# Kernel tuning notes

Measured on AMD Instinct MI355X. Metric: run time of the kernel, lower is better.

The kernel has to match this reference:

```python
import jax, jax.numpy as jnp
import numpy as np

DIM = 1024
HID = 2048
E = 8
K = 2
EPS = 1e-9


def setup_inputs() -> dict:
    key = jax.random.key(0)
    ks = jax.random.split(key, 6)
    scale = 0.02
    return {
        "x": jax.random.normal(ks[0], (4, 2048, DIM), jnp.float32),
        "gate_w": jax.random.normal(ks[1], (DIM, E), jnp.float32) * scale,
        "gate_b": jnp.zeros((E,), jnp.float32),
        # stacked expert weights: leading dim = expert index
        "w1": jax.random.normal(ks[2], (E, DIM, HID), jnp.float32) * scale,
        "b1": jnp.zeros((E, HID), jnp.float32),
        "w2": jax.random.normal(ks[3], (E, DIM, HID), jnp.float32) * scale,
        "b2": jnp.zeros((E, HID), jnp.float32),
        "w3": jax.random.normal(ks[4], (E, HID, DIM), jnp.float32) * scale,
        "b3": jnp.zeros((E, DIM), jnp.float32),
    }


def reference(x, gate_w, gate_b, w1, b1, w2, b2, w3, b3):
    # x: (b, s, d)
    logits = x @ gate_w + gate_b                      # (b, s, E)
    scores = jax.nn.softmax(logits, axis=-1)
    topk_scores, topk_idx = jax.lax.top_k(scores, K)  # (b, s, K)

    usage = scores.mean(axis=(0, 1))                  # (E,)
    load_balance_loss = jnp.sum(usage * jnp.log(usage + EPS))

    # per-expert combine weight: score if expert in top-k else 0  -> (b, s, E)
    onehot = jax.nn.one_hot(topk_idx, E, dtype=x.dtype)            # (b, s, K, E)
    combine = jnp.sum(topk_scores[..., None] * onehot, axis=2)     # (b, s, E)

    out = jnp.zeros_like(x)
    for e in range(E):  # small fixed loop over experts
        gate = jax.nn.sigmoid(x @ w2[e] + b2[e])      # (b, s, H)
        h = (x @ w1[e] + b1[e]) * gate                # SwiGLU hidden
        out = out + combine[..., e:e + 1] * (h @ w3[e] + b3[e])
    return out, load_balance_loss
```

## Files before the change

### kernel.cpp

```cpp
#include <hip/hip_runtime.h>
#include <hip/hip_bf16.h>
#include <math.h>

#define N_TOK 8192
#define DIM   1024
#define HID   2048
#define NE    8
#define NT1   16
#define NT2   32
#define NB1   16
#define NB2   4
#define MAXT  72
#define PANEL1_SH ((size_t)(128 * 256 * 8))
#define PANEL3_SH ((size_t)(256 * 256 * 8))
#define XBLK_SH   ((size_t)(128 * 128 * 8))
#define HBLK_SH   ((size_t)(256 * 128 * 8))

typedef __attribute__((ext_vector_type(8))) short short8;
typedef __attribute__((ext_vector_type(4))) float f32x4;
typedef unsigned short us;

__device__ __forceinline__ us f2bf(float f) {
    unsigned int u = __builtin_bit_cast(unsigned int, f);
    unsigned int r = (u + 0x7fffu + ((u >> 16) & 1u)) >> 16;
    return (us)r;
}

__device__ __forceinline__ float bf2f(us v) {
    unsigned int u = ((unsigned int)v) << 16;
    return __builtin_bit_cast(float, u);
}

__device__ __forceinline__ void gl_lds16(const us* g, us* l) {
    __builtin_amdgcn_global_load_lds(
        (const __attribute__((address_space(1))) void*)g,
        (__attribute__((address_space(3))) void*)l, 16, 0, 0);
}

#define VMW4 asm volatile("s_waitcnt vmcnt(4)" ::: "memory")
#define VMW0 asm volatile("s_waitcnt vmcnt(0)" ::: "memory")
#define BARM asm volatile("s_barrier" ::: "memory")
#define PRIO1 __builtin_amdgcn_s_setprio(1)
#define PRIO0 __builtin_amdgcn_s_setprio(0)

__global__ __launch_bounds__(256) void gate_compute(
    const float* __restrict__ x, const float* __restrict__ gw, const float* __restrict__ gb,
    int* __restrict__ sel, float2* __restrict__ wpair, float* __restrict__ usage_part)
{
    const int lane = threadIdx.x & 63;
    const int tok = blockIdx.x * 4 + (threadIdx.x >> 6);

    __shared__ float su[NE];
    if (threadIdx.x < NE) su[threadIdx.x] = 0.f;
    __syncthreads();

    float acc[NE];
#pragma unroll
    for (int e = 0; e < NE; e++) acc[e] = 0.f;

    const float* xr = x + (size_t)tok * DIM;
    for (int d = lane; d < DIM; d += 64) {
        float xv = xr[d];
        const float4* g4 = (const float4*)(gw + (size_t)d * NE);
        float4 ga = g4[0], gc = g4[1];
        acc[0] = fmaf(xv, ga.x, acc[0]);
        acc[1] = fmaf(xv, ga.y, acc[1]);
        acc[2] = fmaf(xv, ga.z, acc[2]);
        acc[3] = fmaf(xv, ga.w, acc[3]);
        acc[4] = fmaf(xv, gc.x, acc[4]);
        acc[5] = fmaf(xv, gc.y, acc[5]);
        acc[6] = fmaf(xv, gc.z, acc[6]);
        acc[7] = fmaf(xv, gc.w, acc[7]);
    }
#pragma unroll
    for (int e = 0; e < NE; e++) {
#pragma unroll
        for (int off = 32; off > 0; off >>= 1)
            acc[e] += __shfl_xor(acc[e], off);
    }

    if (lane == 0) {
        float lg[NE], p[NE];
        float mx = -1e30f;
#pragma unroll
        for (int e = 0; e < NE; e++) { lg[e] = acc[e] + gb[e]; mx = fmaxf(mx, lg[e]); }
        float s = 0.f;
#pragma unroll
        for (int e = 0; e < NE; e++) { p[e] = __expf(lg[e] - mx); s += p[e]; }
        float inv = 1.f / s;
#pragma unroll
        for (int e = 0; e < NE; e++) p[e] *= inv;
#pragma unroll
        for (int e = 0; e < NE; e++) atomicAdd(&su[e], p[e]);

        int e1 = 0; float v1 = p[0];
#pragma unroll
        for (int e = 1; e < NE; e++) if (p[e] > v1) { v1 = p[e]; e1 = e; }
        int e2 = -1; float v2 = -1e30f;
#pragma unroll
        for (int e = 0; e < NE; e++) if (e != e1 && p[e] > v2) { v2 = p[e]; e2 = e; }

        sel[tok] = e1 | (e2 << 4);
        wpair[tok] = make_float2(v1, v2);
    }
    __syncthreads();
    if (threadIdx.x < NE) usage_part[blockIdx.x * NE + threadIdx.x] = su[threadIdx.x];
}

__global__ __launch_bounds__(256) void scan_kernel(
    const int* __restrict__ sel, const float2* __restrict__ wpair,
    int* __restrict__ counts, int* __restrict__ lists, float* __restrict__ wlist)
{
    const int e = blockIdx.x;
    const int t = threadIdx.x;
    const int base_tok = t * 32;

    unsigned selm = 0, km = 0;
#pragma unroll
    for (int i = 0; i < 32; i++) {
        int s = sel[base_tok + i];
        int e1 = s & 15, e2 = (s >> 4) & 15;
        if (e1 == e) selm |= (1u << i);
        else if (e2 == e) { selm |= (1u << i); km |= (1u << i); }
    }
    const int myc = __popc(selm);

    __shared__ int tot[256];
    tot[t] = myc;
    __syncthreads();
#pragma unroll
    for (int d = 1; d < 256; d <<= 1) {
        int v = (t >= d) ? tot[t - d] : 0;
        __syncthreads();
        tot[t] += v;
        __syncthreads();
    }
    int pos = tot[t] - myc;
    if (t == 255) counts[e] = tot[255];

    for (int i = 0; i < 32; i++) {
        if (selm & (1u << i)) {
            int tok = base_tok + i;
            int k = (km >> i) & 1;
            lists[e * N_TOK + pos] = tok * 2 + k;
            float2 wp = wpair[tok];
            wlist[e * N_TOK + pos] = k ? wp.y : wp.x;
            pos++;
        }
    }
}

__global__ __launch_bounds__(256) void usage_reduce(
    const float* __restrict__ part, float* __restrict__ usage)
{
    const int t = threadIdx.x;
    const int e = t & 7, chunk = t >> 3;
    float s = 0.f;
    for (int b = chunk; b < 2048; b += 32) s += part[b * NE + e];
    __shared__ float red[256];
    red[t] = s;
    __syncthreads();
#pragma unroll
    for (int step = 128; step >= 8; step >>= 1) {
        if (t < step) red[t] += red[t + step];
        __syncthreads();
    }
    if (t < NE) usage[t] = red[t];
}

__global__ void loss_kernel(const float* __restrict__ usage, float* __restrict__ out_loss)
{
    if (threadIdx.x == 0) {
        float l = 0.f;
        for (int e = 0; e < NE; e++) {
            float u = usage[e] / (float)N_TOK;
            l += u * logf(u + 1e-9f);
        }
        *out_loss = l;
    }
}

__global__ void prefix_kernel(const int* __restrict__ counts,
                              int* __restrict__ base_exact, int* __restrict__ ntiles,
                              int* __restrict__ tmap_e, int* __restrict__ tmap_m0)
{
    if (threadIdx.x == 0) {
        int bx = 0, nt = 0;
        for (int e = 0; e < NE; e++) {
            base_exact[e] = bx;
            for (int m0 = 0; m0 < counts[e]; m0 += 256) {
                tmap_e[nt] = e; tmap_m0[nt] = m0; nt++;
            }
            bx += counts[e];
        }
        ntiles[0] = nt;
    }
}

__global__ __launch_bounds__(256) void inv_kernel(
    const int* __restrict__ counts, const int* __restrict__ lists,
    const int* __restrict__ base_exact, int* __restrict__ inv)
{
    const int e = blockIdx.y;
    const int idx = blockIdx.x * 256 + threadIdx.x;
    if (idx < counts[e]) inv[lists[e * N_TOK + idx]] = base_exact[e] + idx;
}

__global__ __launch_bounds__(256) void xgather_kernel(
    const float* __restrict__ x,
    const int* __restrict__ counts, const int* __restrict__ lists,
    const int* __restrict__ base_exact,
    us* __restrict__ Xg)
{
    __shared__ int toks[128];
    __shared__ int bexs[NE], cnts[NE];
    const int t = threadIdx.x;
    if (t < NE) { bexs[t] = base_exact[t]; cnts[t] = counts[t]; }
    __syncthreads();
    if (t < 128) {
        int gpos = blockIdx.x * 128 + t;
        int e = 0;
#pragma unroll
        for (int k = 1; k < NE; k++) if (gpos >= bexs[k]) e = k;
        int idx = gpos - bexs[e];
        int tok = (idx < cnts[e]) ? (lists[e * N_TOK + idx] >> 1) : 0;
        toks[t] = tok;
    }
    __syncthreads();

    us* op = Xg + (size_t)blockIdx.x * XBLK_SH;
    const int rr = t & 127;
    const int ch = t >> 7;
    const int tok = toks[rr];
#pragma unroll
    for (int it = 0; it < 64; it++) {
        int c = it * 2 + ch;
        const float4* src = (const float4*)(x + (size_t)tok * DIM + c * 8);
        float4 a = src[0], b = src[1];
        short8 v;
        v[0] = (short)f2bf(a.x); v[1] = (short)f2bf(a.y);
        v[2] = (short)f2bf(a.z); v[3] = (short)f2bf(a.w);
        v[4] = (short)f2bf(b.x); v[5] = (short)f2bf(b.y);
        v[6] = (short)f2bf(b.z); v[7] = (short)f2bf(b.w);
        *(short8*)(op + (size_t)(c * 128 + rr) * 8) = v;
    }
}

__global__ __launch_bounds__(256) void wswz12_kernel(
    const float* __restrict__ w1, const float* __restrict__ w2, us* __restrict__ out)
{
    const int e = blockIdx.z, nbx = blockIdx.y, gs = blockIdx.x;
    us* op = out + ((size_t)e * NB1 + nbx) * PANEL1_SH + (size_t)gs * 8 * 256 * 8;
    const float* w1e = w1 + (size_t)e * DIM * HID;
    const float* w2e = w2 + (size_t)e * DIM * HID;
    const int t = threadIdx.x;
#pragma unroll
    for (int it = 0; it < 8; it++) {
        int idx = it * 256 + t;
        int g = idx >> 8, row = idx & 255;
        int col = nbx * 128 + (row & 127);
        const float* src = (row < 128 ? w1e : w2e) + (size_t)((gs * 8 + g) * 8) * HID + col;
        short8 v;
#pragma unroll
        for (int s = 0; s < 8; s++) v[s] = (short)f2bf(src[(size_t)s * HID]);
        *(short8*)(op + (size_t)idx * 8) = v;
    }
}

__global__ __launch_bounds__(256) void wswz3_kernel(
    const float* __restrict__ w3, us* __restrict__ out)
{
    const int e = blockIdx.z, nbx = blockIdx.y, gs = blockIdx.x;
    us* op = out + ((size_t)e * NB2 + nbx) * PANEL3_SH + (size_t)gs * 8 * 256 * 8;
    const float* w3e = w3 + (size_t)e * HID * DIM;
    const int t = threadIdx.x;
#pragma unroll
    for (int it = 0; it < 8; it++) {
        int idx = it * 256 + t;
        int g = idx >> 8, row = idx & 255;
        int col = nbx * 256 + row;
        const float* src = w3e + (size_t)((gs * 8 + g) * 8) * DIM + col;
        short8 v;
#pragma unroll
        for (int s = 0; s < 8; s++) v[s] = (short)f2bf(src[(size_t)s * DIM]);
        *(short8*)(op + (size_t)idx * 8) = v;
    }
}

#define ABUF(b) ((us*)(SM + (b)*32768))
#define BBUF(b) ((us*)(SM + 65536 + (b)*32768))

#define AF_READ(b, h) do {                                               \
    _Pragma("unroll")                                                    \
    for (int mi = 0; mi < 8; mi++)                                       \
        af[mi] = *(const short8*)(ABUF(b) + ((h)*1024 + kc*256 + Mw + mi*16 + fr)*8); \
} while (0)
#define BF_READ4(b, h) do {                                              \
    _Pragma("unroll")                                                    \
    for (int j = 0; j < 4; j++)                                          \
        bfv[j] = *(const short8*)(BBUF(b) + ((h)*1024 + kc*256 + Nw + j*16 + fr)*8); \
} while (0)
#define CLUST4 do {                                                      \
    PRIO1;                                                               \
    _Pragma("unroll")                                                    \
    for (int j = 0; j < 4; j++) {                                        \
        _Pragma("unroll")                                                \
        for (int mi = 0; mi < 8; mi++)                                   \
            acc[mi][j] = __builtin_amdgcn_mfma_f32_16x16x32_bf16(        \
                af[mi], bfv[j], acc[mi][j], 0, 0, 0);                    \
    }                                                                    \
    PRIO0;                                                               \
} while (0)

__global__ __launch_bounds__(512, 2) void ffn1_mfma_kernel(
    const us* __restrict__ Xg, const us* __restrict__ W12sw,
    const float* __restrict__ b1, const float* __restrict__ b2,
    const int* __restrict__ counts, const int* __restrict__ base_exact,
    const int* __restrict__ ntiles, const int* __restrict__ tmap_e, const int* __restrict__ tmap_m0,
    us* __restrict__ Hsw)
{
    const int hw = blockIdx.x;
    const int ix = hw >> 3;
    const int nbx = ((hw & 7) << 1) | (ix & 1);
    const int by  = ix >> 1;
    if (by >= ntiles[0]) return;
    const int e  = tmap_e[by];
    const int m0 = tmap_m0[by];
    const int cnt = counts[e];
    const int bex = base_exact[e];

    __shared__ __align__(16) unsigned char SM[132096];

    const int t = threadIdx.x;
    const int lane = t & 63, wv = t >> 6;
    const int wr = wv >> 2, wc = wv & 3;
    const int Mw = wr * 128, Nw = wc * 64;
    const int fr = lane & 15, kc = lane >> 4;

    float bb[4];
    {
        const float* bsrc = (wc < 2) ? b1 : b2;
#pragma unroll
        for (int ni = 0; ni < 4; ni++)
            bb[ni] = bsrc[e * HID + nbx * 128 + (wc & 1) * 64 + ni * 16 + fr];
    }
    __syncthreads();

    const int c0 = wv * 128 + lane;
    const int c1 = c0 + 64;
    const int RA0 = min(bex + m0 + (c0 & 255), N_TOK * 2 - 1);
    const int RA1 = min(bex + m0 + (c1 & 255), N_TOK * 2 - 1);
    const us* ApA = Xg + (size_t)(RA0 >> 7) * XBLK_SH + (size_t)(c0 >> 8) * 1024 + (RA0 & 127) * 8;
    const us* ApB = Xg + (size_t)(RA1 >> 7) * XBLK_SH + (size_t)(c1 >> 8) * 1024 + (RA1 & 127) * 8;
    const us* Wp = W12sw + ((size_t)e * NB1 + nbx) * PANEL1_SH;
    const int dbase = wv * 128 * 8;

    f32x4 acc[8][4];
    const f32x4 fz = {0.f, 0.f, 0.f, 0.f};
#pragma unroll
    for (int i = 0; i < 8; i++)
#pragma unroll
        for (int j = 0; j < 4; j++) acc[i][j] = fz;

    #define STAGE_A(b, tile, h) do {                                             \
        gl_lds16(ApA + (size_t)((tile)*8 + (h)*4) * 1024, ABUF(b) + ((h)*1024)*8 + dbase); \
        gl_lds16(ApB + (size_t)((tile)*8 + (h)*4) * 1024, ABUF(b) + ((h)*1024 + 64)*8 + dbase); \
    } while (0)
    #define STAGE_B(b, tile, h) do {                                             \
        const us* s_ = Wp + ((size_t)(tile)*2048 + (h)*1024) * 8;                \
        gl_lds16(s_ + (size_t)c0 * 8, BBUF(b) + ((h)*1024)*8 + dbase);           \
        gl_lds16(s_ + (size_t)c1 * 8, BBUF(b) + ((h)*1024 + 64)*8 + dbase);      \
    } while (0)

    short8 af[8], bfv[4];

    STAGE_A(0, 0, 0); STAGE_B(0, 0, 0); STAGE_A(0, 0, 1); STAGE_B(0, 0, 1);
    VMW4; BARM;

    for (int tl = 0; tl < NT1; ++tl) {
        const int b = tl & 1, nb = b ^ 1;
        const bool more = (tl + 1 < NT1);
        AF_READ(b, 0); BF_READ4(b, 0);
        if (more) { STAGE_A(nb, tl + 1, 0); STAGE_B(nb, tl + 1, 0); VMW4; } else { VMW0; }
        BARM; CLUST4; BARM;
        AF_READ(b, 1); BF_READ4(b, 1);
        if (more) { STAGE_A(nb, tl + 1, 1); STAGE_B(nb, tl + 1, 1); VMW4; }
        BARM; CLUST4; BARM;
    }
    #undef STAGE_A
    #undef STAGE_B

    float* G = (float*)SM;
    if (wc >= 2) {
        const int cp = wc - 2;
#pragma unroll
        for (int ni = 0; ni < 4; ni++) {
            int c2 = cp * 64 + ni * 16 + fr;
#pragma unroll
            for (int mi = 0; mi < 8; mi++) {
#pragma unroll
                for (int j = 0; j < 4; j++) {
                    int m = mi * 16 + kc * 4 + j;
                    float g = 1.f / (1.f + __expf(-(acc[mi][ni][j] + bb[ni])));
                    G[(wr * 128 + c2) * 129 + m] = g;
                }
            }
        }
    }
    __syncthreads();
    if (wc < 2) {
#pragma unroll
        for (int ni = 0; ni < 4; ni++) {
            int c2 = wc * 64 + ni * 16 + fr;
            int ch = nbx * 128 + c2;
            size_t cb = (size_t)(ch >> 3) * 128 * 8 + (ch & 7);
#pragma unroll
            for (int mi = 0; mi < 8; mi++) {
#pragma unroll
                for (int j = 0; j < 4; j++) {
                    int m = mi * 16 + kc * 4 + j;
                    int rl = wr * 128 + m;
                    if (m0 + rl >= cnt) continue;
                    float h = (acc[mi][ni][j] + bb[ni]) * G[(wr * 128 + c2) * 129 + m];
                    int R = bex + m0 + rl;
                    Hsw[(size_t)(R >> 7) * HBLK_SH + cb + (size_t)(R & 127) * 8] = f2bf(h);
                }
            }
        }
    }
}

__global__ __launch_bounds__(512, 2) void ffn2_mfma_kernel(
    const us* __restrict__ Hsw, const us* __restrict__ W3sw, const float* __restrict__ b3,
    const int* __restrict__ counts, const int* __restrict__ base_exact,
    const int* __restrict__ ntiles, const int* __restrict__ tmap_e, const int* __restrict__ tmap_m0,
    const float* __restrict__ wts,
    us* __restrict__ Pb)
{
    const int hw = blockIdx.x;
    const int xcd = hw & 7;
    const int ix = hw >> 3;
    const int nbx = xcd & 3;
    const int by = (ix << 1) | (xcd >> 2);
    if (by >= ntiles[0]) return;
    const int e  = tmap_e[by];
    const int m0 = tmap_m0[by];
    const int cnt = counts[e];
    const int bex = base_exact[e];

    __shared__ __align__(16) unsigned char SM[132096];
    float* rowwt = (float*)(SM + 131072);

    const int t = threadIdx.x;
    if (t < 256) {
        int idx = m0 + t;
        rowwt[t] = (idx < cnt) ? wts[e * N_TOK + idx] : 0.f;
    }

    const int lane = t & 63, wv = t >> 6;
    const int wr = wv >> 2, wc = wv & 3;
    const int Mw = wr * 128, Nw = wc * 64;
    const int fr = lane & 15, kc = lane >> 4;

    float bb3[4];
#pragma unroll
    for (int ni = 0; ni < 4; ni++)
        bb3[ni] = b3[e * DIM + nbx * 256 + wc * 64 + ni * 16 + fr];
    __syncthreads();

    const int c0 = wv * 128 + lane;
    const int c1 = c0 + 64;
    const int RA0 = min(bex + m0 + (c0 & 255), N_TOK * 2 - 1);
    const int RA1 = min(bex + m0 + (c1 & 255), N_TOK * 2 - 1);
    const us* HpA = Hsw + (size_t)(RA0 >> 7) * HBLK_SH + (size_t)(c0 >> 8) * 1024 + (RA0 & 127) * 8;
    const us* HpB = Hsw + (size_t)(RA1 >> 7) * HBLK_SH + (size_t)(c1 >> 8) * 1024 + (RA1 & 127) * 8;
    const us* Wp = W3sw + ((size_t)e * NB2 + nbx) * PANEL3_SH;
    const int dbase = wv * 128 * 8;

    f32x4 acc[8][4];
    const f32x4 fz = {0.f, 0.f, 0.f, 0.f};
#pragma unroll
    for (int i = 0; i < 8; i++)
#pragma unroll
        for (int j = 0; j < 4; j++) acc[i][j] = fz;

    #define STAGE_A2(b, tile, h) do {                                            \
        gl_lds16(HpA + (size_t)((tile)*8 + (h)*4) * 1024, ABUF(b) + ((h)*1024)*8 + dbase); \
        gl_lds16(HpB + (size_t)((tile)*8 + (h)*4) * 1024, ABUF(b) + ((h)*1024 + 64)*8 + dbase); \
    } while (0)
    #define STAGE_B2(b, tile, h) do {                                            \
        const us* s_ = Wp + ((size_t)(tile)*2048 + (h)*1024) * 8;                \
        gl_lds16(s_ + (size_t)c0 * 8, BBUF(b) + ((h)*1024)*8 + dbase);           \
        gl_lds16(s_ + (size_t)c1 * 8, BBUF(b) + ((h)*1024 + 64)*8 + dbase);      \
    } while (0)

    short8 af[8], bfv[4];

    STAGE_A2(0, 0, 0); STAGE_B2(0, 0, 0); STAGE_A2(0, 0, 1); STAGE_B2(0, 0, 1);
    VMW4; BARM;

    for (int tl = 0; tl < NT2; ++tl) {
        const int b = tl & 1, nb = b ^ 1;
        const bool more = (tl + 1 < NT2);
        AF_READ(b, 0); BF_READ4(b, 0);
        if (more) { STAGE_A2(nb, tl + 1, 0); STAGE_B2(nb, tl + 1, 0); VMW4; } else { VMW0; }
        BARM; CLUST4; BARM;
        AF_READ(b, 1); BF_READ4(b, 1);
        if (more) { STAGE_A2(nb, tl + 1, 1); STAGE_B2(nb, tl + 1, 1); VMW4; }
        BARM; CLUST4; BARM;
    }
    #undef STAGE_A2
    #undef STAGE_B2

#pragma unroll
    for (int ni = 0; ni < 4; ni++) {
        int col = nbx * 256 + wc * 64 + ni * 16 + fr;
#pragma unroll
        for (int mi = 0; mi < 8; mi++) {
#pragma unroll
            for (int j = 0; j < 4; j++) {
                int rl = wr * 128 + mi * 16 + kc * 4 + j;
                if (m0 + rl >= cnt) continue;
                float v = (acc[mi][ni][j] + bb3[ni]) * rowwt[rl];
                Pb[(size_t)(bex + m0 + rl) * DIM + col] = f2bf(v);
            }
        }
    }
}

__global__ __launch_bounds__(256) void combine_kernel(
    const us* __restrict__ Pb, const int* __restrict__ inv,
    float* __restrict__ out)
{
    int gid = blockIdx.x * 256 + threadIdx.x;
    int tok = gid >> 7;
    int c8 = (gid & 127) * 8;
    const short8 a = *(const short8*)(Pb + (size_t)inv[tok * 2] * DIM + c8);
    const short8 b = *(const short8*)(Pb + (size_t)inv[tok * 2 + 1] * DIM + c8);
    float4 r0, r1;
    r0.x = bf2f((us)a[0]) + bf2f((us)b[0]);
    r0.y = bf2f((us)a[1]) + bf2f((us)b[1]);
    r0.z = bf2f((us)a[2]) + bf2f((us)b[2]);
    r0.w = bf2f((us)a[3]) + bf2f((us)b[3]);
    r1.x = bf2f((us)a[4]) + bf2f((us)b[4]);
    r1.y = bf2f((us)a[5]) + bf2f((us)b[5]);
    r1.z = bf2f((us)a[6]) + bf2f((us)b[6]);
    r1.w = bf2f((us)a[7]) + bf2f((us)b[7]);
    float* o = out + (size_t)tok * DIM + c8;
    *(float4*)o = r0;
    *(float4*)(o + 4) = r1;
}

extern "C" void kernel_launch(void* const* d_in, const int* in_sizes, int n_in,
                              void* d_out, int out_size, void* d_ws, size_t ws_size,
                              hipStream_t stream) {
    (void)in_sizes; (void)n_in; (void)out_size; (void)ws_size;
    const float* x      = (const float*)d_in[0];
    const float* gate_w = (const float*)d_in[1];
    const float* gate_b = (const float*)d_in[2];
    const float* w1     = (const float*)d_in[3];
    const float* b1     = (const float*)d_in[4];
    const float* w2     = (const float*)d_in[5];
    const float* b2     = (const float*)d_in[6];
    const float* w3     = (const float*)d_in[7];
    const float* b3     = (const float*)d_in[8];
    float* out = (float*)d_out;

    char* ws = (char*)d_ws;
    float* usage      = (float*)ws;
    int*   counts     = (int*)(ws + 32);
    int*   base_exact = (int*)(ws + 64);
    int*   ntiles     = (int*)(ws + 96);
    int*   tmap_e     = (int*)(ws + 128);
    int*   tmap_m0    = (int*)(ws + 640);
    int*   lists      = (int*)(ws + 4096);
    float* wts        = (float*)(ws + 4096 + (size_t)NE * N_TOK * 4);
    int*   inv        = (int*)(ws + 4096 + (size_t)2 * NE * N_TOK * 4);
    int*   sel        = (int*)(ws + 4096 + 576 * 1024);
    float2* wpair     = (float2*)(ws + 4096 + 608 * 1024);
    float* usage_part = (float*)(ws + 4096 + 672 * 1024);
    us* Hsw   = (us*)(ws + (1ull  << 20));
    us* W12sw = (us*)(ws + (65ull << 20));
    us* W3sw  = W12sw;
    us* Pb    = (us*)(ws + (97ull << 20));
    us* Xg    = (us*)d_out;

    gate_compute<<<N_TOK / 4, 256, 0, stream>>>(x, gate_w, gate_b, sel, wpair, usage_part);
    scan_kernel<<<NE, 256, 0, stream>>>(sel, wpair, counts, lists, wts);
    usage_reduce<<<1, 256, 0, stream>>>(usage_part, usage);
    prefix_kernel<<<1, 64, 0, stream>>>(counts, base_exact, ntiles, tmap_e, tmap_m0);
    {
        dim3 gI(N_TOK / 256, NE);
        inv_kernel<<<gI, 256, 0, stream>>>(counts, lists, base_exact, inv);
    }
    xgather_kernel<<<N_TOK * 2 / 128, 256, 0, stream>>>(x, counts, lists, base_exact, Xg);

    dim3 gW12(16, NB1, NE);
    wswz12_kernel<<<gW12, 256, 0, stream>>>(w1, w2, W12sw);

    ffn1_mfma_kernel<<<NB1 * MAXT, 512, 0, stream>>>(Xg, W12sw, b1, b2, counts, base_exact,
                                                     ntiles, tmap_e, tmap_m0, Hsw);

    loss_kernel<<<1, 64, 0, stream>>>(usage, out + (size_t)N_TOK * DIM);

    dim3 gW3(32, NB2, NE);
    wswz3_kernel<<<gW3, 256, 0, stream>>>(w3, W3sw);

    ffn2_mfma_kernel<<<4 * MAXT, 512, 0, stream>>>(Hsw, W3sw, b3, counts, base_exact,
                                                   ntiles, tmap_e, tmap_m0, wts, Pb);
    combine_kernel<<<N_TOK * 128 / 256, 256, 0, stream>>>(Pb, inv, out);
}
```

Baseline: 502.2 us.

## Shrink expert GEMM tiles to 128x128 with fused dual-weight FFN1 and bf16 x pre-cast

Both expert GEMMs now use 128-row by 128-column tiles with 256-thread blocks and a simple double-buffered K loop, replacing 256x256 tiles with 512 threads. FFN1 computes the w1 and w2 products together in one block and applies SwiGLU in registers, so the LDS round trip for the gate values goes away. The gate kernel also writes a bf16 copy of x, so the gather only copies data instead of converting it. Smaller tiles mean more blocks and less per-block padding waste, but operand reuse per LDS load drops and each K step now ends with a full vmcnt(0) wait and a barrier.

```diff
diff --git a/kernel.cpp b/kernel.cpp
--- a/kernel.cpp
+++ b/kernel.cpp
@@ -6,13 +6,13 @@
 #define DIM   1024
 #define HID   2048
 #define NE    8
-#define NT1   16
-#define NT2   32
-#define NB1   16
-#define NB2   4
-#define MAXT  72
-#define PANEL1_SH ((size_t)(128 * 256 * 8))
-#define PANEL3_SH ((size_t)(256 * 256 * 8))
+#define NK1   32
+#define NK2   64
+#define NP1   16
+#define NP2   8
+#define MAXT  136
+#define PANEL_SH  ((size_t)(128 * 128 * 8))
+#define PANEL3_SH ((size_t)(256 * 128 * 8))
 #define XBLK_SH   ((size_t)(128 * 128 * 8))
 #define HBLK_SH   ((size_t)(256 * 128 * 8))
 
@@ -25,19 +25,16 @@
     unsigned int r = (u + 0x7fffu + ((u >> 16) & 1u)) >> 16;
     return (us)r;
 }
-
 __device__ __forceinline__ float bf2f(us v) {
     unsigned int u = ((unsigned int)v) << 16;
     return __builtin_bit_cast(float, u);
 }
-
 __device__ __forceinline__ void gl_lds16(const us* g, us* l) {
     __builtin_amdgcn_global_load_lds(
         (const __attribute__((address_space(1))) void*)g,
         (__attribute__((address_space(3))) void*)l, 16, 0, 0);
 }
 
-#define VMW4 asm volatile("s_waitcnt vmcnt(4)" ::: "memory")
 #define VMW0 asm volatile("s_waitcnt vmcnt(0)" ::: "memory")
 #define BARM asm volatile("s_barrier" ::: "memory")
 #define PRIO1 __builtin_amdgcn_s_setprio(1)
@@ -45,7 +42,8 @@
 
 __global__ __launch_bounds__(256) void gate_compute(
     const float* __restrict__ x, const float* __restrict__ gw, const float* __restrict__ gb,
-    int* __restrict__ sel, float2* __restrict__ wpair, float* __restrict__ usage_part)
+    int* __restrict__ sel, float2* __restrict__ wpair, float* __restrict__ usage_part,
+    us* __restrict__ xb)
 {
     const int lane = threadIdx.x & 63;
     const int tok = blockIdx.x * 4 + (threadIdx.x >> 6);
@@ -59,8 +57,10 @@
     for (int e = 0; e < NE; e++) acc[e] = 0.f;
 
     const float* xr = x + (size_t)tok * DIM;
+    us* xbr = xb + (size_t)tok * DIM;
     for (int d = lane; d < DIM; d += 64) {
         float xv = xr[d];
+        xbr[d] = f2bf(xv);
         const float4* g4 = (const float4*)(gw + (size_t)d * NE);
         float4 ga = g4[0], gc = g4[1];
         acc[0] = fmaf(xv, ga.x, acc[0]);
@@ -188,7 +188,7 @@
         int bx = 0, nt = 0;
         for (int e = 0; e < NE; e++) {
             base_exact[e] = bx;
-            for (int m0 = 0; m0 < counts[e]; m0 += 256) {
+            for (int m0 = 0; m0 < counts[e]; m0 += 128) {
                 tmap_e[nt] = e; tmap_m0[nt] = m0; nt++;
             }
             bx += counts[e];
@@ -207,7 +207,7 @@
 }
 
 __global__ __launch_bounds__(256) void xgather_kernel(
-    const float* __restrict__ x,
+    const us* __restrict__ Xbf,
     const int* __restrict__ counts, const int* __restrict__ lists,
     const int* __restrict__ base_exact,
     us* __restrict__ Xg)
@@ -231,35 +231,30 @@
     us* op = Xg + (size_t)blockIdx.x * XBLK_SH;
     const int rr = t & 127;
     const int ch = t >> 7;
-    const int tok = toks[rr];
+    const us* srcrow = Xbf + (size_t)toks[rr] * DIM;
 #pragma unroll
     for (int it = 0; it < 64; it++) {
         int c = it * 2 + ch;
-        const float4* src = (const float4*)(x + (size_t)tok * DIM + c * 8);
-        float4 a = src[0], b = src[1];
-        short8 v;
-        v[0] = (short)f2bf(a.x); v[1] = (short)f2bf(a.y);
-        v[2] = (short)f2bf(a.z); v[3] = (short)f2bf(a.w);
-        v[4] = (short)f2bf(b.x); v[5] = (short)f2bf(b.y);
-        v[6] = (short)f2bf(b.z); v[7] = (short)f2bf(b.w);
+        short8 v = *(const short8*)(srcrow + c * 8);
         *(short8*)(op + (size_t)(c * 128 + rr) * 8) = v;
     }
 }
 
 __global__ __launch_bounds__(256) void wswz12_kernel(
-    const float* __restrict__ w1, const float* __restrict__ w2, us* __restrict__ out)
-{
-    const int e = blockIdx.z, nbx = blockIdx.y, gs = blockIdx.x;
-    us* op = out + ((size_t)e * NB1 + nbx) * PANEL1_SH + (size_t)gs * 8 * 256 * 8;
-    const float* w1e = w1 + (size_t)e * DIM * HID;
-    const float* w2e = w2 + (size_t)e * DIM * HID;
-    const int t = threadIdx.x;
-#pragma unroll
-    for (int it = 0; it < 8; it++) {
+    const float* __restrict__ w1, const float* __restrict__ w2,
+    us* __restrict__ o1, us* __restrict__ o2)
+{
+    const int ez = blockIdx.z;
+    const int which = ez & 1, e = ez >> 1;
+    const int nbx = blockIdx.y, gs = blockIdx.x;
+    const float* we = (which ? w2 : w1) + (size_t)e * DIM * HID;
+    us* op = (which ? o2 : o1) + ((size_t)e * NP1 + nbx) * PANEL_SH + (size_t)gs * 8 * 1024;
+    const int t = threadIdx.x;
+#pragma unroll
+    for (int it = 0; it < 4; it++) {
         int idx = it * 256 + t;
-        int g = idx >> 8, row = idx & 255;
-        int col = nbx * 128 + (row & 127);
-        const float* src = (row < 128 ? w1e : w2e) + (size_t)((gs * 8 + g) * 8) * HID + col;
+        int g_local = idx >> 7, row = idx & 127;
+        const float* src = we + (size_t)((gs * 8 + g_local) * 8) * HID + nbx * 128 + row;
         short8 v;
 #pragma unroll
         for (int s = 0; s < 8; s++) v[s] = (short)f2bf(src[(size_t)s * HID]);
@@ -271,15 +266,14 @@
     const float* __restrict__ w3, us* __restrict__ out)
 {
     const int e = blockIdx.z, nbx = blockIdx.y, gs = blockIdx.x;
-    us* op = out + ((size_t)e * NB2 + nbx) * PANEL3_SH + (size_t)gs * 8 * 256 * 8;
-    const float* w3e = w3 + (size_t)e * HID * DIM;
-    const int t = threadIdx.x;
-#pragma unroll
-    for (int it = 0; it < 8; it++) {
+    const float* we = w3 + (size_t)e * HID * DIM;
+    us* op = out + ((size_t)e * NP2 + nbx) * PANEL3_SH + (size_t)gs * 8 * 1024;
+    const int t = threadIdx.x;
+#pragma unroll
+    for (int it = 0; it < 4; it++) {
         int idx = it * 256 + t;
-        int g = idx >> 8, row = idx & 255;
-        int col = nbx * 256 + row;
-        const float* src = w3e + (size_t)((gs * 8 + g) * 8) * DIM + col;
+        int g_local = idx >> 7, row = idx & 127;
+        const float* src = we + (size_t)((gs * 8 + g_local) * 8) * DIM + nbx * 128 + row;
         short8 v;
 #pragma unroll
         for (int s = 0; s < 8; s++) v[s] = (short)f2bf(src[(size_t)s * DIM]);
@@ -287,33 +281,9 @@
     }
 }
 
-#define ABUF(b) ((us*)(SM + (b)*32768))
-#define BBUF(b) ((us*)(SM + 65536 + (b)*32768))
-
-#define AF_READ(b, h) do {                                               \
-    _Pragma("unroll")                                                    \
-    for (int mi = 0; mi < 8; mi++)                                       \
-        af[mi] = *(const short8*)(ABUF(b) + ((h)*1024 + kc*256 + Mw + mi*16 + fr)*8); \
-} while (0)
-#define BF_READ4(b, h) do {                                              \
-    _Pragma("unroll")                                                    \
-    for (int j = 0; j < 4; j++)                                          \
-        bfv[j] = *(const short8*)(BBUF(b) + ((h)*1024 + kc*256 + Nw + j*16 + fr)*8); \
-} while (0)
-#define CLUST4 do {                                                      \
-    PRIO1;                                                               \
-    _Pragma("unroll")                                                    \
-    for (int j = 0; j < 4; j++) {                                        \
-        _Pragma("unroll")                                                \
-        for (int mi = 0; mi < 8; mi++)                                   \
-            acc[mi][j] = __builtin_amdgcn_mfma_f32_16x16x32_bf16(        \
-                af[mi], bfv[j], acc[mi][j], 0, 0, 0);                    \
-    }                                                                    \
-    PRIO0;                                                               \
-} while (0)
-
-__global__ __launch_bounds__(512, 2) void ffn1_mfma_kernel(
-    const us* __restrict__ Xg, const us* __restrict__ W12sw,
+__global__ __launch_bounds__(256) void ffn1_mfma_kernel(
+    const us* __restrict__ Xg,
+    const us* __restrict__ W1sw, const us* __restrict__ W2sw,
     const float* __restrict__ b1, const float* __restrict__ b2,
     const int* __restrict__ counts, const int* __restrict__ base_exact,
     const int* __restrict__ ntiles, const int* __restrict__ tmap_e, const int* __restrict__ tmap_m0,
@@ -329,108 +299,99 @@
     const int cnt = counts[e];
     const int bex = base_exact[e];
 
-    __shared__ __align__(16) unsigned char SM[132096];
+    __shared__ __align__(16) us As[2][4096];
+    __shared__ __align__(16) us B1s[2][4096];
+    __shared__ __align__(16) us B2s[2][4096];
 
     const int t = threadIdx.x;
     const int lane = t & 63, wv = t >> 6;
-    const int wr = wv >> 2, wc = wv & 3;
-    const int Mw = wr * 128, Nw = wc * 64;
+    const int wm = (wv >> 1) * 64, wn = (wv & 1) * 64;
     const int fr = lane & 15, kc = lane >> 4;
 
-    float bb[4];
-    {
-        const float* bsrc = (wc < 2) ? b1 : b2;
+    float bb1[4], bb2[4];
+#pragma unroll
+    for (int ni = 0; ni < 4; ni++) {
+        int ch = nbx * 128 + wn + ni * 16 + fr;
+        bb1[ni] = b1[e * HID + ch];
+        bb2[ni] = b2[e * HID + ch];
+    }
+
+    const int arow = t & 127, akq = t >> 7;
+    const int RA = min(bex + m0 + arow, N_TOK * 2 - 1);
+    const us* Ap  = Xg + (size_t)(RA >> 7) * XBLK_SH + (RA & 127) * 8 + akq * 1024;
+    const us* W1p = W1sw + ((size_t)e * NP1 + nbx) * PANEL_SH + arow * 8 + akq * 1024;
+    const us* W2p = W2sw + ((size_t)e * NP1 + nbx) * PANEL_SH + arow * 8 + akq * 1024;
+    const int d0 = (t & ~63) * 8;
+    const int d1 = d0 + 256 * 8;
+
+    f32x4 acc1[4][4], acc2[4][4];
+    const f32x4 fz = {0.f, 0.f, 0.f, 0.f};
+#pragma unroll
+    for (int i = 0; i < 4; i++)
+#pragma unroll
+        for (int j = 0; j < 4; j++) { acc1[i][j] = fz; acc2[i][j] = fz; }
+
+    #define F1_STAGE(b, ks) do {                                   \
+        const size_t o = (size_t)(ks) * 4096;                      \
+        gl_lds16(Ap  + o,        As[b]  + d0);                     \
+        gl_lds16(Ap  + o + 2048, As[b]  + d1);                     \
+        gl_lds16(W1p + o,        B1s[b] + d0);                     \
+        gl_lds16(W1p + o + 2048, B1s[b] + d1);                     \
+        gl_lds16(W2p + o,        B2s[b] + d0);                     \
+        gl_lds16(W2p + o + 2048, B2s[b] + d1);                     \
+    } while (0)
+
+    short8 af[4], b1v[4], b2v[4];
+
+    F1_STAGE(0, 0);
+    VMW0; BARM;
+
+    for (int ks = 0; ks < NK1; ++ks) {
+        const int b = ks & 1, nb = b ^ 1;
+        if (ks + 1 < NK1) F1_STAGE(nb, ks + 1);
+#pragma unroll
+        for (int mi = 0; mi < 4; mi++)
+            af[mi] = *(const short8*)(As[b] + (kc * 128 + wm + mi * 16 + fr) * 8);
+#pragma unroll
+        for (int ni = 0; ni < 4; ni++) {
+            b1v[ni] = *(const short8*)(B1s[b] + (kc * 128 + wn + ni * 16 + fr) * 8);
+            b2v[ni] = *(const short8*)(B2s[b] + (kc * 128 + wn + ni * 16 + fr) * 8);
+        }
+        PRIO1;
 #pragma unroll
         for (int ni = 0; ni < 4; ni++)
-            bb[ni] = bsrc[e * HID + nbx * 128 + (wc & 1) * 64 + ni * 16 + fr];
-    }
-    __syncthreads();
-
-    const int c0 = wv * 128 + lane;
-    const int c1 = c0 + 64;
-    const int RA0 = min(bex + m0 + (c0 & 255), N_TOK * 2 - 1);
-    const int RA1 = min(bex + m0 + (c1 & 255), N_TOK * 2 - 1);
-    const us* ApA = Xg + (size_t)(RA0 >> 7) * XBLK_SH + (size_t)(c0 >> 8) * 1024 + (RA0 & 127) * 8;
-    const us* ApB = Xg + (size_t)(RA1 >> 7) * XBLK_SH + (size_t)(c1 >> 8) * 1024 + (RA1 & 127) * 8;
-    const us* Wp = W12sw + ((size_t)e * NB1 + nbx) * PANEL1_SH;
-    const int dbase = wv * 128 * 8;
-
-    f32x4 acc[8][4];
-    const f32x4 fz = {0.f, 0.f, 0.f, 0.f};
-#pragma unroll
-    for (int i = 0; i < 8; i++)
-#pragma unroll
-        for (int j = 0; j < 4; j++) acc[i][j] = fz;
-
-    #define STAGE_A(b, tile, h) do {                                             \
-        gl_lds16(ApA + (size_t)((tile)*8 + (h)*4) * 1024, ABUF(b) + ((h)*1024)*8 + dbase); \
-        gl_lds16(ApB + (size_t)((tile)*8 + (h)*4) * 1024, ABUF(b) + ((h)*1024 + 64)*8 + dbase); \
-    } while (0)
-    #define STAGE_B(b, tile, h) do {                                             \
-        const us* s_ = Wp + ((size_t)(tile)*2048 + (h)*1024) * 8;                \
-        gl_lds16(s_ + (size_t)c0 * 8, BBUF(b) + ((h)*1024)*8 + dbase);           \
-        gl_lds16(s_ + (size_t)c1 * 8, BBUF(b) + ((h)*1024 + 64)*8 + dbase);      \
-    } while (0)
-
-    short8 af[8], bfv[4];
-
-    STAGE_A(0, 0, 0); STAGE_B(0, 0, 0); STAGE_A(0, 0, 1); STAGE_B(0, 0, 1);
-    VMW4; BARM;
-
-    for (int tl = 0; tl < NT1; ++tl) {
-        const int b = tl & 1, nb = b ^ 1;
-        const bool more = (tl + 1 < NT1);
-        AF_READ(b, 0); BF_READ4(b, 0);
-        if (more) { STAGE_A(nb, tl + 1, 0); STAGE_B(nb, tl + 1, 0); VMW4; } else { VMW0; }
-        BARM; CLUST4; BARM;
-        AF_READ(b, 1); BF_READ4(b, 1);
-        if (more) { STAGE_A(nb, tl + 1, 1); STAGE_B(nb, tl + 1, 1); VMW4; }
-        BARM; CLUST4; BARM;
-    }
-    #undef STAGE_A
-    #undef STAGE_B
-
-    float* G = (float*)SM;
-    if (wc >= 2) {
-        const int cp = wc - 2;
-#pragma unroll
-        for (int ni = 0; ni < 4; ni++) {
-            int c2 = cp * 64 + ni * 16 + fr;
-#pragma unroll
-            for (int mi = 0; mi < 8; mi++) {
-#pragma unroll
-                for (int j = 0; j < 4; j++) {
-                    int m = mi * 16 + kc * 4 + j;
-                    float g = 1.f / (1.f + __expf(-(acc[mi][ni][j] + bb[ni])));
-                    G[(wr * 128 + c2) * 129 + m] = g;
-                }
+#pragma unroll
+            for (int mi = 0; mi < 4; mi++) {
+                acc1[mi][ni] = __builtin_amdgcn_mfma_f32_16x16x32_bf16(af[mi], b1v[ni], acc1[mi][ni], 0, 0, 0);
+                acc2[mi][ni] = __builtin_amdgcn_mfma_f32_16x16x32_bf16(af[mi], b2v[ni], acc2[mi][ni], 0, 0, 0);
+            }
+        PRIO0;
+        VMW0;
+        BARM;
+    }
+    #undef F1_STAGE
+
+#pragma unroll
+    for (int ni = 0; ni < 4; ni++) {
+        int ch = nbx * 128 + wn + ni * 16 + fr;
+        size_t cb = (size_t)(ch >> 3) * 1024 + (ch & 7);
+#pragma unroll
+        for (int mi = 0; mi < 4; mi++) {
+#pragma unroll
+            for (int j = 0; j < 4; j++) {
+                int m = wm + mi * 16 + kc * 4 + j;
+                if (m0 + m >= cnt) continue;
+                float v1 = acc1[mi][ni][j] + bb1[ni];
+                float v2 = acc2[mi][ni][j] + bb2[ni];
+                float h = v1 * (1.f / (1.f + __expf(-v2)));
+                int R = bex + m0 + m;
+                Hsw[(size_t)(R >> 7) * HBLK_SH + cb + (size_t)(R & 127) * 8] = f2bf(h);
             }
         }
     }
-    __syncthreads();
-    if (wc < 2) {
-#pragma unroll
-        for (int ni = 0; ni < 4; ni++) {
-            int c2 = wc * 64 + ni * 16 + fr;
-            int ch = nbx * 128 + c2;
-            size_t cb = (size_t)(ch >> 3) * 128 * 8 + (ch & 7);
-#pragma unroll
-            for (int mi = 0; mi < 8; mi++) {
-#pragma unroll
-                for (int j = 0; j < 4; j++) {
-                    int m = mi * 16 + kc * 4 + j;
-                    int rl = wr * 128 + m;
-                    if (m0 + rl >= cnt) continue;
-                    float h = (acc[mi][ni][j] + bb[ni]) * G[(wr * 128 + c2) * 129 + m];
-                    int R = bex + m0 + rl;
-                    Hsw[(size_t)(R >> 7) * HBLK_SH + cb + (size_t)(R & 127) * 8] = f2bf(h);
-                }
-            }
-        }
-    }
-}
-
-__global__ __launch_bounds__(512, 2) void ffn2_mfma_kernel(
+}
+
+__global__ __launch_bounds__(256) void ffn2_mfma_kernel(
     const us* __restrict__ Hsw, const us* __restrict__ W3sw, const float* __restrict__ b3,
     const int* __restrict__ counts, const int* __restrict__ base_exact,
     const int* __restrict__ ntiles, const int* __restrict__ tmap_e, const int* __restrict__ tmap_m0,
@@ -438,91 +399,92 @@
     us* __restrict__ Pb)
 {
     const int hw = blockIdx.x;
-    const int xcd = hw & 7;
-    const int ix = hw >> 3;
-    const int nbx = xcd & 3;
-    const int by = (ix << 1) | (xcd >> 2);
+    const int nbx = hw & 7;
+    const int by = hw >> 3;
     if (by >= ntiles[0]) return;
     const int e  = tmap_e[by];
     const int m0 = tmap_m0[by];
     const int cnt = counts[e];
     const int bex = base_exact[e];
 
-    __shared__ __align__(16) unsigned char SM[132096];
-    float* rowwt = (float*)(SM + 131072);
-
-    const int t = threadIdx.x;
-    if (t < 256) {
+    __shared__ __align__(16) us As[2][4096];
+    __shared__ __align__(16) us B3s[2][4096];
+    __shared__ float rowwt[128];
+
+    const int t = threadIdx.x;
+    if (t < 128) {
         int idx = m0 + t;
         rowwt[t] = (idx < cnt) ? wts[e * N_TOK + idx] : 0.f;
     }
 
     const int lane = t & 63, wv = t >> 6;
-    const int wr = wv >> 2, wc = wv & 3;
-    const int Mw = wr * 128, Nw = wc * 64;
+    const int wm = (wv >> 1) * 64, wn = (wv & 1) * 64;
     const int fr = lane & 15, kc = lane >> 4;
 
     float bb3[4];
 #pragma unroll
     for (int ni = 0; ni < 4; ni++)
-        bb3[ni] = b3[e * DIM + nbx * 256 + wc * 64 + ni * 16 + fr];
-    __syncthreads();
-
-    const int c0 = wv * 128 + lane;
-    const int c1 = c0 + 64;
-    const int RA0 = min(bex + m0 + (c0 & 255), N_TOK * 2 - 1);
-    const int RA1 = min(bex + m0 + (c1 & 255), N_TOK * 2 - 1);
-    const us* HpA = Hsw + (size_t)(RA0 >> 7) * HBLK_SH + (size_t)(c0 >> 8) * 1024 + (RA0 & 127) * 8;
-    const us* HpB = Hsw + (size_t)(RA1 >> 7) * HBLK_SH + (size_t)(c1 >> 8) * 1024 + (RA1 & 127) * 8;
-    const us* Wp = W3sw + ((size_t)e * NB2 + nbx) * PANEL3_SH;
-    const int dbase = wv * 128 * 8;
-
-    f32x4 acc[8][4];
+        bb3[ni] = b3[e * DIM + nbx * 128 + wn + ni * 16 + fr];
+
+    const int arow = t & 127, akq = t >> 7;
+    const int RA = min(bex + m0 + arow, N_TOK * 2 - 1);
+    const us* Hp  = Hsw + (size_t)(RA >> 7) * HBLK_SH + (RA & 127) * 8 + akq * 1024;
+    const us* W3p = W3sw + ((size_t)e * NP2 + nbx) * PANEL3_SH + arow * 8 + akq * 1024;
+    const int d0 = (t & ~63) * 8;
+    const int d1 = d0 + 256 * 8;
+
+    f32x4 acc[4][4];
     const f32x4 fz = {0.f, 0.f, 0.f, 0.f};
 #pragma unroll
-    for (int i = 0; i < 8; i++)
+    for (int i = 0; i < 4; i++)
 #pragma unroll
         for (int j = 0; j < 4; j++) acc[i][j] = fz;
 
-    #define STAGE_A2(b, tile, h) do {                                            \
-        gl_lds16(HpA + (size_t)((tile)*8 + (h)*4) * 1024, ABUF(b) + ((h)*1024)*8 + dbase); \
-        gl_lds16(HpB + (size_t)((tile)*8 + (h)*4) * 1024, ABUF(b) + ((h)*1024 + 64)*8 + dbase); \
+    #define F2_STAGE(b, ks) do {                                   \
+        const size_t o = (size_t)(ks) * 4096;                      \
+        gl_lds16(Hp  + o,        As[b]  + d0);                     \
+        gl_lds16(Hp  + o + 2048, As[b]  + d1);                     \
+        gl_lds16(W3p + o,        B3s[b] + d0);                     \
+        gl_lds16(W3p + o + 2048, B3s[b] + d1);                     \
     } while (0)
-    #define STAGE_B2(b, tile, h) do {                                            \
-        const us* s_ = Wp + ((size_t)(tile)*2048 + (h)*1024) * 8;                \
-        gl_lds16(s_ + (size_t)c0 * 8, BBUF(b) + ((h)*1024)*8 + dbase);           \
-        gl_lds16(s_ + (size_t)c1 * 8, BBUF(b) + ((h)*1024 + 64)*8 + dbase);      \
-    } while (0)
-
-    short8 af[8], bfv[4];
-
-    STAGE_A2(0, 0, 0); STAGE_B2(0, 0, 0); STAGE_A2(0, 0, 1); STAGE_B2(0, 0, 1);
-    VMW4; BARM;
-
-    for (int tl = 0; tl < NT2; ++tl) {
-        const int b = tl & 1, nb = b ^ 1;
-        const bool more = (tl + 1 < NT2);
-        AF_READ(b, 0); BF_READ4(b, 0);
-        if (more) { STAGE_A2(nb, tl + 1, 0); STAGE_B2(nb, tl + 1, 0); VMW4; } else { VMW0; }
-        BARM; CLUST4; BARM;
-        AF_READ(b, 1); BF_READ4(b, 1);
-        if (more) { STAGE_A2(nb, tl + 1, 1); STAGE_B2(nb, tl + 1, 1); VMW4; }
-        BARM; CLUST4; BARM;
-    }
-    #undef STAGE_A2
-    #undef STAGE_B2
+
+    short8 af[4], b3v[4];
+
+    F2_STAGE(0, 0);
+    VMW0; BARM;
+
+    for (int ks = 0; ks < NK2; ++ks) {
+        const int b = ks & 1, nb = b ^ 1;
+        if (ks + 1 < NK2) F2_STAGE(nb, ks + 1);
+#pragma unroll
+        for (int mi = 0; mi < 4; mi++)
+            af[mi] = *(const short8*)(As[b] + (kc * 128 + wm + mi * 16 + fr) * 8);
+#pragma unroll
+        for (int ni = 0; ni < 4; ni++)
+            b3v[ni] = *(const short8*)(B3s[b] + (kc * 128 + wn + ni * 16 + fr) * 8);
+        PRIO1;
+#pragma unroll
+        for (int ni = 0; ni < 4; ni++)
+#pragma unroll
+            for (int mi = 0; mi < 4; mi++)
+                acc[mi][ni] = __builtin_amdgcn_mfma_f32_16x16x32_bf16(af[mi], b3v[ni], acc[mi][ni], 0, 0, 0);
+        PRIO0;
+        VMW0;
+        BARM;
+    }
+    #undef F2_STAGE
 
 #pragma unroll
     for (int ni = 0; ni < 4; ni++) {
-        int col = nbx * 256 + wc * 64 + ni * 16 + fr;
-#pragma unroll
-        for (int mi = 0; mi < 8; mi++) {
+        int col = nbx * 128 + wn + ni * 16 + fr;
+#pragma unroll
+        for (int mi = 0; mi < 4; mi++) {
 #pragma unroll
             for (int j = 0; j < 4; j++) {
-                int rl = wr * 128 + mi * 16 + kc * 4 + j;
-                if (m0 + rl >= cnt) continue;
-                float v = (acc[mi][ni][j] + bb3[ni]) * rowwt[rl];
-                Pb[(size_t)(bex + m0 + rl) * DIM + col] = f2bf(v);
+                int m = wm + mi * 16 + kc * 4 + j;
+                if (m0 + m >= cnt) continue;
+                float v = (acc[mi][ni][j] + bb3[ni]) * rowwt[m];
+                Pb[(size_t)(bex + m0 + m) * DIM + col] = f2bf(v);
             }
         }
     }
@@ -572,7 +534,7 @@
     int*   base_exact = (int*)(ws + 64);
     int*   ntiles     = (int*)(ws + 96);
     int*   tmap_e     = (int*)(ws + 128);
-    int*   tmap_m0    = (int*)(ws + 640);
+    int*   tmap_m0    = (int*)(ws + 1152);
     int*   lists      = (int*)(ws + 4096);
     float* wts        = (float*)(ws + 4096 + (size_t)NE * N_TOK * 4);
     int*   inv        = (int*)(ws + 4096 + (size_t)2 * NE * N_TOK * 4);
@@ -580,12 +542,14 @@
     float2* wpair     = (float2*)(ws + 4096 + 608 * 1024);
     float* usage_part = (float*)(ws + 4096 + 672 * 1024);
     us* Hsw   = (us*)(ws + (1ull  << 20));
-    us* W12sw = (us*)(ws + (65ull << 20));
-    us* W3sw  = W12sw;
+    us* W1sw  = (us*)(ws + (65ull << 20));
+    us* W2sw  = (us*)(ws + (97ull << 20));
+    us* W3sw  = W1sw;
     us* Pb    = (us*)(ws + (97ull << 20));
+    us* Xbf   = (us*)(ws + (97ull << 20));
     us* Xg    = (us*)d_out;
 
-    gate_compute<<<N_TOK / 4, 256, 0, stream>>>(x, gate_w, gate_b, sel, wpair, usage_part);
+    gate_compute<<<N_TOK / 4, 256, 0, stream>>>(x, gate_w, gate_b, sel, wpair, usage_part, Xbf);
     scan_kernel<<<NE, 256, 0, stream>>>(sel, wpair, counts, lists, wts);
     usage_reduce<<<1, 256, 0, stream>>>(usage_part, usage);
     prefix_kernel<<<1, 64, 0, stream>>>(counts, base_exact, ntiles, tmap_e, tmap_m0);
@@ -593,20 +557,20 @@
         dim3 gI(N_TOK / 256, NE);
         inv_kernel<<<gI, 256, 0, stream>>>(counts, lists, base_exact, inv);
     }
-    xgather_kernel<<<N_TOK * 2 / 128, 256, 0, stream>>>(x, counts, lists, base_exact, Xg);
-
-    dim3 gW12(16, NB1, NE);
-    wswz12_kernel<<<gW12, 256, 0, stream>>>(w1, w2, W12sw);
-
-    ffn1_mfma_kernel<<<NB1 * MAXT, 512, 0, stream>>>(Xg, W12sw, b1, b2, counts, base_exact,
-                                                     ntiles, tmap_e, tmap_m0, Hsw);
+    xgather_kernel<<<N_TOK * 2 / 128, 256, 0, stream>>>(Xbf, counts, lists, base_exact, Xg);
+
+    dim3 gW12(16, NP1, NE * 2);
+    wswz12_kernel<<<gW12, 256, 0, stream>>>(w1, w2, W1sw, W2sw);
+
+    ffn1_mfma_kernel<<<16 * MAXT, 256, 0, stream>>>(Xg, W1sw, W2sw, b1, b2,
+                                                    counts, base_exact, ntiles, tmap_e, tmap_m0, Hsw);
 
     loss_kernel<<<1, 64, 0, stream>>>(usage, out + (size_t)N_TOK * DIM);
 
-    dim3 gW3(32, NB2, NE);
+    dim3 gW3(32, NP2, NE);
     wswz3_kernel<<<gW3, 256, 0, stream>>>(w3, W3sw);
 
-    ffn2_mfma_kernel<<<4 * MAXT, 512, 0, stream>>>(Hsw, W3sw, b3, counts, base_exact,
-                                                   ntiles, tmap_e, tmap_m0, wts, Pb);
+    ffn2_mfma_kernel<<<8 * MAXT, 256, 0, stream>>>(Hsw, W3sw, b3,
+                                                   counts, base_exact, ntiles, tmap_e, tmap_m0, wts, Pb);
     combine_kernel<<<N_TOK * 128 / 256, 256, 0, stream>>>(Pb, inv, out);
 }
```

Result: slower. 593.0 us (+18.1%).
